# Optimization experiments

Hardware: AMD Instinct MI355X
Metric: run time of the kernel (lower is better)

## Reference

```python
import jax, jax.numpy as jnp
import numpy as np

B, S, D, F, E = 8, 4096, 512, 2048, 8


def setup_inputs() -> dict:
    key = jax.random.key(0)
    ks = jax.random.split(key, 10)
    std = 0.02
    return {
        "x": jax.random.normal(ks[0], (B, S, D), dtype=jnp.float32),
        "gate_w": jax.random.normal(ks[1], (D, E), dtype=jnp.float32) * std,
        "gate_b": jnp.zeros((E,), dtype=jnp.float32),
        "w1": jax.random.normal(ks[2], (E, D, F), dtype=jnp.float32) * std,
        "b1": jnp.zeros((E, F), dtype=jnp.float32),
        "w2": jax.random.normal(ks[3], (E, D, F), dtype=jnp.float32) * std,
        "b2": jnp.zeros((E, F), dtype=jnp.float32),
        "w3": jax.random.normal(ks[4], (E, F, D), dtype=jnp.float32) * std,
        "b3": jnp.zeros((E, D), dtype=jnp.float32),
    }


def reference(x, gate_w, gate_b, w1, b1, w2, b2, w3, b3):
    b, s, d = x.shape
    xt = x.reshape(-1, d)                      # [N, D]
    logits = xt @ gate_w + gate_b              # [N, E]
    top = jnp.argmax(logits, axis=-1)          # [N] top-1 expert per token
    soft = jax.nn.softmax(logits, axis=-1)     # [N, E]
    num_experts = gate_w.shape[1]

    out = jnp.zeros_like(xt)
    # Loop over the small fixed expert set; weight is zero where a token
    # is not routed to expert i, reproducing masked dispatch+combine math.
    for i in range(num_experts):
        h = jax.nn.gelu(xt @ w1[i] + b1[i], approximate=False) * (xt @ w2[i] + b2[i])
        y = h @ w3[i] + b3[i]                  # [N, D]
        w = jnp.where(top == i, soft[:, i], 0.0)[:, None]
        out = out + w * y

    aux_loss = jnp.asarray(0.0, dtype=x.dtype)  # eval mode: no aux loss
    return out.reshape(b, s, d), aux_loss
```

## Files before the change

kernel.cpp:

```cpp
#include <hip/hip_runtime.h>
#include <hip/hip_bf16.h>

typedef unsigned short u16;
typedef __bf16 bf16x8 __attribute__((ext_vector_type(8)));
typedef float f32x4 __attribute__((ext_vector_type(4)));

#define N_TOK 32768
#define DD 512
#define FF 2048
#define EE 8

#define CTL_CNT 0
#define CTL_CUR 8
#define CTL_OFF 16
#define CTL_NT 25
#define CTL_TE 32
#define CTL_TI 304

__device__ inline u16 f2bu(float f) {
  unsigned u = __builtin_bit_cast(unsigned, f);
  unsigned r = (u + 0x7fffu + ((u >> 16) & 1u)) >> 16;
  return (u16)r;
}

__device__ inline f32x4 mfma16(bf16x8 a, bf16x8 b, f32x4 c) {
  return __builtin_amdgcn_mfma_f32_16x16x32_bf16(a, b, c, 0, 0, 0);
}

__device__ inline void gload_lds16(const void* g, void* l) {
  __builtin_amdgcn_global_load_lds(
      (const __attribute__((address_space(1))) void*)g,
      (__attribute__((address_space(3))) void*)l, 16, 0, 0);
}

__device__ inline void stage128x32(u16* lds, const u16* g, int ld) {
  const int t = threadIdx.x;
#pragma unroll
  for (int s = 0; s < 2; ++s) {
    const int e = s * 2048 + t * 8;
    const int row = e >> 5;
    const int kin = e & 31;
    gload_lds16(g + (size_t)row * ld + kin, lds + e);
  }
}

__global__ void gate_k(const float* __restrict__ x, const float* __restrict__ gw,
                       const float* __restrict__ gb, int* __restrict__ eid,
                       float* __restrict__ wgt) {
  __shared__ float gws[DD * EE];
  for (int i = threadIdx.x; i < DD * EE; i += 256) gws[i] = gw[i];
  __syncthreads();
  const int tok = (int)((blockIdx.x * 256 + threadIdx.x) >> 6);
  const int lane = threadIdx.x & 63;
  const float* xr = x + (size_t)tok * DD;
  float a[EE];
#pragma unroll
  for (int e = 0; e < EE; ++e) a[e] = 0.f;
#pragma unroll
  for (int i = 0; i < 8; ++i) {
    const int d = lane + i * 64;
    const float xv = xr[d];
#pragma unroll
    for (int e = 0; e < EE; ++e) a[e] += xv * gws[d * EE + e];
  }
#pragma unroll
  for (int e = 0; e < EE; ++e) {
#pragma unroll
    for (int off = 32; off > 0; off >>= 1) a[e] += __shfl_xor(a[e], off);
  }
  if (lane == 0) {
    float m = -1e30f; int bi = 0;
#pragma unroll
    for (int e = 0; e < EE; ++e) {
      const float l2 = a[e] + gb[e];
      a[e] = l2;
      if (l2 > m) { m = l2; bi = e; }
    }
    float s = 0.f;
#pragma unroll
    for (int e = 0; e < EE; ++e) s += expf(a[e] - m);
    eid[tok] = bi;
    wgt[tok] = 1.f / s;
  }
}

__global__ void count_k(const int* __restrict__ eid, int* __restrict__ ctl) {
  __shared__ int h[EE];
  if (threadIdx.x < EE) h[threadIdx.x] = 0;
  __syncthreads();
  atomicAdd(&h[eid[blockIdx.x * 256 + threadIdx.x]], 1);
  __syncthreads();
  if (threadIdx.x < EE) atomicAdd(&ctl[CTL_CNT + threadIdx.x], h[threadIdx.x]);
}

__global__ void scan_k(int* __restrict__ ctl, float* __restrict__ aux) {
  int o = 0, nt = 0;
  for (int e = 0; e < EE; ++e) {
    ctl[CTL_OFF + e] = o;
    ctl[CTL_CUR + e] = o;
    const int c = ctl[CTL_CNT + e];
    const int t = (c + 127) >> 7;
    for (int i = 0; i < t; ++i) { ctl[CTL_TE + nt] = e; ctl[CTL_TI + nt] = i; ++nt; }
    o += c;
  }
  ctl[CTL_OFF + 8] = o;
  ctl[CTL_NT] = nt;
  *aux = 0.f;
}

__global__ void pos_k(const int* __restrict__ eid, const float* __restrict__ wgt,
                      int* __restrict__ ctl, int* __restrict__ sorted,
                      float* __restrict__ wgt_s) {
  __shared__ int h[EE], base[EE];
  const int t = blockIdx.x * 256 + threadIdx.x;
  if (threadIdx.x < EE) h[threadIdx.x] = 0;
  __syncthreads();
  const int e = eid[t];
  const int r = atomicAdd(&h[e], 1);
  __syncthreads();
  if (threadIdx.x < EE)
    base[threadIdx.x] = atomicAdd(&ctl[CTL_CUR + threadIdx.x], h[threadIdx.x]);
  __syncthreads();
  const int p = base[e] + r;
  sorted[p] = t;
  wgt_s[p] = wgt[t];
}

__global__ void gather_k(const float* __restrict__ x, const int* __restrict__ sorted,
                         u16* __restrict__ Xg) {
  const int p = (int)((blockIdx.x * 256 + threadIdx.x) >> 6);
  const int lane = threadIdx.x & 63;
  const int t = sorted[p];
  const float* src = x + (size_t)t * DD + lane * 8;
  const float4 v0 = *(const float4*)(src);
  const float4 v1 = *(const float4*)(src + 4);
  union { u16 u[8]; uint4 v; } o;
  o.u[0] = f2bu(v0.x); o.u[1] = f2bu(v0.y); o.u[2] = f2bu(v0.z); o.u[3] = f2bu(v0.w);
  o.u[4] = f2bu(v1.x); o.u[5] = f2bu(v1.y); o.u[6] = f2bu(v1.z); o.u[7] = f2bu(v1.w);
  *reinterpret_cast<uint4*>(Xg + (size_t)p * DD + lane * 8) = o.v;
}

__global__ void transp_k(const float* __restrict__ in, u16* __restrict__ out,
                         int R, int C) {
  __shared__ u16 tile[64][66];
  const int e = blockIdx.z;
  const int c0 = blockIdx.x * 64, r0 = blockIdx.y * 64;
  const float* ip = in + (size_t)e * R * C;
  u16* op = out + (size_t)e * R * C;
  const int tx = threadIdx.x & 63, ty = threadIdx.x >> 6;
#pragma unroll
  for (int k = 0; k < 16; ++k) {
    const int r = ty * 16 + k;
    tile[r][tx] = f2bu(ip[(size_t)(r0 + r) * C + c0 + tx]);
  }
  __syncthreads();
#pragma unroll
  for (int k = 0; k < 16; ++k) {
    const int c = ty * 16 + k;
    op[(size_t)(c0 + c) * R + r0 + tx] = tile[tx][c];
  }
}

__global__ __launch_bounds__(256, 2) void gemm1_k(
    const u16* __restrict__ Xg, const u16* __restrict__ W1t,
    const u16* __restrict__ W2t, const float* __restrict__ b1,
    const float* __restrict__ b2, u16* __restrict__ Hbuf,
    const int* __restrict__ ctl) {
  const int bx = blockIdx.x;
  if (bx >= ctl[CTL_NT]) return;
  const int e = ctl[CTL_TE + bx];
  const int ti = ctl[CTL_TI + bx];
  const int cnt = ctl[CTL_CNT + e];
  const int row0 = ctl[CTL_OFF + e] + ti * 128;
  const int rows = min(128, cnt - ti * 128);
  const int n0 = blockIdx.y * 128;

  __shared__ u16 As[2][4096];
  __shared__ u16 B1s[2][4096];
  __shared__ u16 B2s[2][4096];

  const u16* Ab = Xg + (size_t)row0 * DD;
  const u16* B1b = W1t + ((size_t)e * FF + n0) * DD;
  const u16* B2b = W2t + ((size_t)e * FF + n0) * DD;

  const f32x4 z = {0.f, 0.f, 0.f, 0.f};
  f32x4 acc1[4][4], acc2[4][4];
#pragma unroll
  for (int i = 0; i < 4; ++i)
#pragma unroll
    for (int j = 0; j < 4; ++j) { acc1[i][j] = z; acc2[i][j] = z; }

  stage128x32(As[0], Ab, DD);
  stage128x32(B1s[0], B1b, DD);
  stage128x32(B2s[0], B2b, DD);
  asm volatile("s_waitcnt vmcnt(0)" ::: "memory");
  __syncthreads();

  const int lane = threadIdx.x & 63;
  const int w = threadIdx.x >> 6;
  const int wr = w >> 1, wc = w & 1;
  const int ro = (lane & 15) * 32 + (lane >> 4) * 8;

  int cur = 0;
  for (int kt = 0; kt < 16; ++kt) {
    if (kt < 15) {
      stage128x32(As[cur ^ 1], Ab + (kt + 1) * 32, DD);
      stage128x32(B1s[cur ^ 1], B1b + (kt + 1) * 32, DD);
      stage128x32(B2s[cur ^ 1], B2b + (kt + 1) * 32, DD);
    }
    bf16x8 af[4], bf1[4], bf2[4];
#pragma unroll
    for (int mi = 0; mi < 4; ++mi)
      af[mi] = *(const bf16x8*)&As[cur][(wr * 64 + mi * 16) * 32 + ro];
#pragma unroll
    for (int ni = 0; ni < 4; ++ni) {
      bf1[ni] = *(const bf16x8*)&B1s[cur][(wc * 64 + ni * 16) * 32 + ro];
      bf2[ni] = *(const bf16x8*)&B2s[cur][(wc * 64 + ni * 16) * 32 + ro];
    }
#pragma unroll
    for (int mi = 0; mi < 4; ++mi)
#pragma unroll
      for (int ni = 0; ni < 4; ++ni) {
        acc1[mi][ni] = mfma16(af[mi], bf1[ni], acc1[mi][ni]);
        acc2[mi][ni] = mfma16(af[mi], bf2[ni], acc2[mi][ni]);
      }
    asm volatile("s_waitcnt vmcnt(0)" ::: "memory");
    __syncthreads();
    cur ^= 1;
  }

#pragma unroll
  for (int mi = 0; mi < 4; ++mi) {
#pragma unroll
    for (int ni = 0; ni < 4; ++ni) {
      const int c = wc * 64 + ni * 16 + (lane & 15);
      const float bb1 = b1[(size_t)e * FF + n0 + c];
      const float bb2 = b2[(size_t)e * FF + n0 + c];
#pragma unroll
      for (int j = 0; j < 4; ++j) {
        const int r = wr * 64 + mi * 16 + (lane >> 4) * 4 + j;
        if (r < rows) {
          const float v1 = acc1[mi][ni][j] + bb1;
          const float v2 = acc2[mi][ni][j] + bb2;
          const float h = 0.5f * v1 * (1.f + erff(v1 * 0.70710678118f)) * v2;
          Hbuf[(size_t)(row0 + r) * FF + n0 + c] = f2bu(h);
        }
      }
    }
  }
}

__global__ __launch_bounds__(256, 2) void gemm2_k(
    const u16* __restrict__ Hbuf, const u16* __restrict__ W3t,
    const float* __restrict__ b3, const int* __restrict__ sorted,
    const float* __restrict__ wgt_s, float* __restrict__ out,
    const int* __restrict__ ctl) {
  const int bx = blockIdx.x;
  if (bx >= ctl[CTL_NT]) return;
  const int e = ctl[CTL_TE + bx];
  const int ti = ctl[CTL_TI + bx];
  const int cnt = ctl[CTL_CNT + e];
  const int row0 = ctl[CTL_OFF + e] + ti * 128;
  const int rows = min(128, cnt - ti * 128);
  const int n0 = blockIdx.y * 128;

  __shared__ u16 As[2][4096];
  __shared__ u16 Bs[2][4096];
  const u16* Ab = Hbuf + (size_t)row0 * FF;
  const u16* Bb = W3t + ((size_t)e * DD + n0) * FF;

  const f32x4 z = {0.f, 0.f, 0.f, 0.f};
  f32x4 acc[4][4];
#pragma unroll
  for (int i = 0; i < 4; ++i)
#pragma unroll
    for (int j = 0; j < 4; ++j) acc[i][j] = z;

  stage128x32(As[0], Ab, FF);
  stage128x32(Bs[0], Bb, FF);
  asm volatile("s_waitcnt vmcnt(0)" ::: "memory");
  __syncthreads();

  const int lane = threadIdx.x & 63;
  const int w = threadIdx.x >> 6;
  const int wr = w >> 1, wc = w & 1;
  const int ro = (lane & 15) * 32 + (lane >> 4) * 8;

  int cur = 0;
  for (int kt = 0; kt < 64; ++kt) {
    if (kt < 63) {
      stage128x32(As[cur ^ 1], Ab + (kt + 1) * 32, FF);
      stage128x32(Bs[cur ^ 1], Bb + (kt + 1) * 32, FF);
    }
    bf16x8 af[4], bf[4];
#pragma unroll
    for (int mi = 0; mi < 4; ++mi)
      af[mi] = *(const bf16x8*)&As[cur][(wr * 64 + mi * 16) * 32 + ro];
#pragma unroll
    for (int ni = 0; ni < 4; ++ni)
      bf[ni] = *(const bf16x8*)&Bs[cur][(wc * 64 + ni * 16) * 32 + ro];
#pragma unroll
    for (int mi = 0; mi < 4; ++mi)
#pragma unroll
      for (int ni = 0; ni < 4; ++ni)
        acc[mi][ni] = mfma16(af[mi], bf[ni], acc[mi][ni]);
    asm volatile("s_waitcnt vmcnt(0)" ::: "memory");
    __syncthreads();
    cur ^= 1;
  }

#pragma unroll
  for (int mi = 0; mi < 4; ++mi) {
#pragma unroll
    for (int ni = 0; ni < 4; ++ni) {
      const int c = wc * 64 + ni * 16 + (lane & 15);
      const float bb3 = b3[(size_t)e * DD + n0 + c];
#pragma unroll
      for (int j = 0; j < 4; ++j) {
        const int r = wr * 64 + mi * 16 + (lane >> 4) * 4 + j;
        if (r < rows) {
          const int p = row0 + r;
          const int tok = sorted[p];
          out[(size_t)tok * DD + n0 + c] = wgt_s[p] * (acc[mi][ni][j] + bb3);
        }
      }
    }
  }
}

extern "C" void kernel_launch(void* const* d_in, const int* in_sizes, int n_in,
                              void* d_out, int out_size, void* d_ws, size_t ws_size,
                              hipStream_t stream) {
  const float* x  = (const float*)d_in[0];
  const float* gw = (const float*)d_in[1];
  const float* gb = (const float*)d_in[2];
  const float* w1 = (const float*)d_in[3];
  const float* b1 = (const float*)d_in[4];
  const float* w2 = (const float*)d_in[5];
  const float* b2 = (const float*)d_in[6];
  const float* w3 = (const float*)d_in[7];
  const float* b3 = (const float*)d_in[8];
  float* out = (float*)d_out;

  char* base = (char*)d_ws;
  size_t off = 0;
  auto take = [&](size_t bytes) {
    char* r = base + off;
    off += (bytes + 255) & ~(size_t)255;
    return r;
  };
  int*   ctl    = (int*)take(4096);
  int*   eid    = (int*)take((size_t)N_TOK * 4);
  float* wgt    = (float*)take((size_t)N_TOK * 4);
  int*   sorted = (int*)take((size_t)(N_TOK + 128) * 4);
  float* wgt_s  = (float*)take((size_t)(N_TOK + 128) * 4);
  u16*   Xg     = (u16*)take((size_t)(N_TOK + 128) * DD * 2);
  u16*   W1t    = (u16*)take((size_t)EE * FF * DD * 2);
  u16*   W2t    = (u16*)take((size_t)EE * FF * DD * 2);
  u16*   W3t    = (u16*)take((size_t)EE * DD * FF * 2);
  u16*   Hbuf   = (u16*)take((size_t)(N_TOK + 128) * FF * 2);

  hipMemsetAsync(ctl, 0, 64, stream);

  gate_k<<<8192, 256, 0, stream>>>(x, gw, gb, eid, wgt);
  count_k<<<128, 256, 0, stream>>>(eid, ctl);
  scan_k<<<1, 1, 0, stream>>>(ctl, out + (size_t)N_TOK * DD);
  pos_k<<<128, 256, 0, stream>>>(eid, wgt, ctl, sorted, wgt_s);
  gather_k<<<8192, 256, 0, stream>>>(x, sorted, Xg);

  transp_k<<<dim3(32, 8, EE), 256, 0, stream>>>(w1, W1t, 512, 2048);
  transp_k<<<dim3(32, 8, EE), 256, 0, stream>>>(w2, W2t, 512, 2048);
  transp_k<<<dim3(8, 32, EE), 256, 0, stream>>>(w3, W3t, 2048, 512);

  gemm1_k<<<dim3(264, 16), 256, 0, stream>>>(Xg, W1t, W2t, b1, b2, Hbuf, ctl);
  gemm2_k<<<dim3(264, 4), 256, 0, stream>>>(Hbuf, W3t, b3, sorted, wgt_s, out, ctl);
}
```

Before: 664.1 us.

## Fuse bf16 cast into gate, gather rows in GEMM, swizzle LDS tiles

The fp32-to-bf16 conversion of x now happens inside the gate kernel, which removes the separate gather kernel. gemm1 instead indexes rows through the sorted permutation while staging its A tiles. Both GEMMs use an XOR-swizzled LDS layout, paired with remapped global-load addresses, to cut bank conflicts on the bf16x8 fragment reads. The gate weights in shared memory are padded to stride 9, and the tile table in scan is built in parallel across 256 threads. The trade-off is that gemm1 now reads scattered rows, giving less coalescing on its A loads.

```diff
diff --git a/kernel.cpp b/kernel.cpp
--- a/kernel.cpp
+++ b/kernel.cpp
@@ -33,26 +33,25 @@
       (__attribute__((address_space(3))) void*)l, 16, 0, 0);
 }
 
-__device__ inline void stage128x32(u16* lds, const u16* g, int ld) {
-  const int t = threadIdx.x;
-#pragma unroll
-  for (int s = 0; s < 2; ++s) {
-    const int e = s * 2048 + t * 8;
-    const int row = e >> 5;
-    const int kin = e & 31;
-    gload_lds16(g + (size_t)row * ld + kin, lds + e);
-  }
-}
 
 __global__ void gate_k(const float* __restrict__ x, const float* __restrict__ gw,
                        const float* __restrict__ gb, int* __restrict__ eid,
-                       float* __restrict__ wgt) {
-  __shared__ float gws[DD * EE];
-  for (int i = threadIdx.x; i < DD * EE; i += 256) gws[i] = gw[i];
+                       float* __restrict__ wgt, u16* __restrict__ Xb) {
+  __shared__ float gws[DD * 9];
+  for (int i = threadIdx.x; i < DD * EE; i += 256)
+    gws[(i >> 3) * 9 + (i & 7)] = gw[i];
   __syncthreads();
   const int tok = (int)((blockIdx.x * 256 + threadIdx.x) >> 6);
   const int lane = threadIdx.x & 63;
   const float* xr = x + (size_t)tok * DD;
+
+  const float4 v0 = *(const float4*)(xr + lane * 8);
+  const float4 v1 = *(const float4*)(xr + lane * 8 + 4);
+  union { u16 u[8]; uint4 v; } o;
+  o.u[0] = f2bu(v0.x); o.u[1] = f2bu(v0.y); o.u[2] = f2bu(v0.z); o.u[3] = f2bu(v0.w);
+  o.u[4] = f2bu(v1.x); o.u[5] = f2bu(v1.y); o.u[6] = f2bu(v1.z); o.u[7] = f2bu(v1.w);
+  *reinterpret_cast<uint4*>(Xb + (size_t)tok * DD + lane * 8) = o.v;
+
   float a[EE];
 #pragma unroll
   for (int e = 0; e < EE; ++e) a[e] = 0.f;
@@ -61,7 +60,7 @@
     const int d = lane + i * 64;
     const float xv = xr[d];
 #pragma unroll
-    for (int e = 0; e < EE; ++e) a[e] += xv * gws[d * EE + e];
+    for (int e = 0; e < EE; ++e) a[e] += xv * gws[d * 9 + e];
   }
 #pragma unroll
   for (int e = 0; e < EE; ++e) {
@@ -94,18 +93,30 @@
 }
 
 __global__ void scan_k(int* __restrict__ ctl, float* __restrict__ aux) {
-  int o = 0, nt = 0;
-  for (int e = 0; e < EE; ++e) {
-    ctl[CTL_OFF + e] = o;
-    ctl[CTL_CUR + e] = o;
-    const int c = ctl[CTL_CNT + e];
-    const int t = (c + 127) >> 7;
-    for (int i = 0; i < t; ++i) { ctl[CTL_TE + nt] = e; ctl[CTL_TI + nt] = i; ++nt; }
-    o += c;
-  }
-  ctl[CTL_OFF + 8] = o;
-  ctl[CTL_NT] = nt;
-  *aux = 0.f;
+  __shared__ int tstart[EE + 1];
+  if (threadIdx.x == 0) {
+    int o = 0, nt = 0;
+    for (int e = 0; e < EE; ++e) {
+      ctl[CTL_OFF + e] = o;
+      ctl[CTL_CUR + e] = o;
+      tstart[e] = nt;
+      const int c = ctl[CTL_CNT + e];
+      nt += (c + 127) >> 7;
+      o += c;
+    }
+    tstart[EE] = nt;
+    ctl[CTL_OFF + 8] = o;
+    ctl[CTL_NT] = nt;
+    *aux = 0.f;
+  }
+  __syncthreads();
+  const int nt = tstart[EE];
+  for (int i = threadIdx.x; i < nt; i += 256) {
+    int e = 0;
+    while (tstart[e + 1] <= i) ++e;
+    ctl[CTL_TE + i] = e;
+    ctl[CTL_TI + i] = i - tstart[e];
+  }
 }
 
 __global__ void pos_k(const int* __restrict__ eid, const float* __restrict__ wgt,
@@ -124,20 +135,6 @@
   const int p = base[e] + r;
   sorted[p] = t;
   wgt_s[p] = wgt[t];
-}
-
-__global__ void gather_k(const float* __restrict__ x, const int* __restrict__ sorted,
-                         u16* __restrict__ Xg) {
-  const int p = (int)((blockIdx.x * 256 + threadIdx.x) >> 6);
-  const int lane = threadIdx.x & 63;
-  const int t = sorted[p];
-  const float* src = x + (size_t)t * DD + lane * 8;
-  const float4 v0 = *(const float4*)(src);
-  const float4 v1 = *(const float4*)(src + 4);
-  union { u16 u[8]; uint4 v; } o;
-  o.u[0] = f2bu(v0.x); o.u[1] = f2bu(v0.y); o.u[2] = f2bu(v0.z); o.u[3] = f2bu(v0.w);
-  o.u[4] = f2bu(v1.x); o.u[5] = f2bu(v1.y); o.u[6] = f2bu(v1.z); o.u[7] = f2bu(v1.w);
-  *reinterpret_cast<uint4*>(Xg + (size_t)p * DD + lane * 8) = o.v;
 }
 
 __global__ void transp_k(const float* __restrict__ in, u16* __restrict__ out,
@@ -162,10 +159,10 @@
 }
 
 __global__ __launch_bounds__(256, 2) void gemm1_k(
-    const u16* __restrict__ Xg, const u16* __restrict__ W1t,
+    const u16* __restrict__ Xb, const u16* __restrict__ W1t,
     const u16* __restrict__ W2t, const float* __restrict__ b1,
     const float* __restrict__ b2, u16* __restrict__ Hbuf,
-    const int* __restrict__ ctl) {
+    const int* __restrict__ sorted, const int* __restrict__ ctl) {
   const int bx = blockIdx.x;
   if (bx >= ctl[CTL_NT]) return;
   const int e = ctl[CTL_TE + bx];
@@ -179,10 +176,32 @@
   __shared__ u16 B1s[2][4096];
   __shared__ u16 B2s[2][4096];
 
-  const u16* Ab = Xg + (size_t)row0 * DD;
   const u16* B1b = W1t + ((size_t)e * FF + n0) * DD;
   const u16* B2b = W2t + ((size_t)e * FF + n0) * DD;
 
+  const int t = threadIdx.x;
+  const u16 *aSrc[2], *b1Src[2], *b2Src[2];
+  int dofs[2];
+#pragma unroll
+  for (int s = 0; s < 2; ++s) {
+    const int Gp = s * 256 + t;
+    const int r = ((Gp >> 3) << 1) | (((Gp >> 2) ^ (Gp >> 4)) & 1);
+    const int g = (Gp & 3) ^ (r & 3);
+    dofs[s] = Gp * 8;
+    const int idx = min(row0 + r, N_TOK - 1);
+    aSrc[s]  = Xb + (size_t)sorted[idx] * DD + g * 8;
+    b1Src[s] = B1b + (size_t)r * DD + g * 8;
+    b2Src[s] = B2b + (size_t)r * DD + g * 8;
+  }
+  auto stage_all = [&](int buf, int kc) {
+#pragma unroll
+    for (int s = 0; s < 2; ++s) gload_lds16(aSrc[s] + kc, &As[buf][dofs[s]]);
+#pragma unroll
+    for (int s = 0; s < 2; ++s) gload_lds16(b1Src[s] + kc, &B1s[buf][dofs[s]]);
+#pragma unroll
+    for (int s = 0; s < 2; ++s) gload_lds16(b2Src[s] + kc, &B2s[buf][dofs[s]]);
+  };
+
   const f32x4 z = {0.f, 0.f, 0.f, 0.f};
   f32x4 acc1[4][4], acc2[4][4];
 #pragma unroll
@@ -190,32 +209,32 @@
 #pragma unroll
     for (int j = 0; j < 4; ++j) { acc1[i][j] = z; acc2[i][j] = z; }
 
-  stage128x32(As[0], Ab, DD);
-  stage128x32(B1s[0], B1b, DD);
-  stage128x32(B2s[0], B2b, DD);
+  stage_all(0, 0);
   asm volatile("s_waitcnt vmcnt(0)" ::: "memory");
   __syncthreads();
 
   const int lane = threadIdx.x & 63;
-  const int w = threadIdx.x >> 6;
+  const int w = t >> 6;
   const int wr = w >> 1, wc = w & 1;
-  const int ro = (lane & 15) * 32 + (lane >> 4) * 8;
+  const int l15 = lane & 15, g8 = (lane >> 4) * 8, xv = (lane & 7) << 3;
+  int offA[4], offB[4];
+#pragma unroll
+  for (int i = 0; i < 4; ++i) {
+    offA[i] = (((wr * 64 + i * 16 + l15) * 32 + g8) ^ xv);
+    offB[i] = (((wc * 64 + i * 16 + l15) * 32 + g8) ^ xv);
+  }
 
   int cur = 0;
   for (int kt = 0; kt < 16; ++kt) {
-    if (kt < 15) {
-      stage128x32(As[cur ^ 1], Ab + (kt + 1) * 32, DD);
-      stage128x32(B1s[cur ^ 1], B1b + (kt + 1) * 32, DD);
-      stage128x32(B2s[cur ^ 1], B2b + (kt + 1) * 32, DD);
-    }
+    if (kt < 15) stage_all(cur ^ 1, (kt + 1) * 32);
     bf16x8 af[4], bf1[4], bf2[4];
 #pragma unroll
     for (int mi = 0; mi < 4; ++mi)
-      af[mi] = *(const bf16x8*)&As[cur][(wr * 64 + mi * 16) * 32 + ro];
+      af[mi] = *(const bf16x8*)&As[cur][offA[mi]];
 #pragma unroll
     for (int ni = 0; ni < 4; ++ni) {
-      bf1[ni] = *(const bf16x8*)&B1s[cur][(wc * 64 + ni * 16) * 32 + ro];
-      bf2[ni] = *(const bf16x8*)&B2s[cur][(wc * 64 + ni * 16) * 32 + ro];
+      bf1[ni] = *(const bf16x8*)&B1s[cur][offB[ni]];
+      bf2[ni] = *(const bf16x8*)&B2s[cur][offB[ni]];
     }
 #pragma unroll
     for (int mi = 0; mi < 4; ++mi)
@@ -269,6 +288,25 @@
   const u16* Ab = Hbuf + (size_t)row0 * FF;
   const u16* Bb = W3t + ((size_t)e * DD + n0) * FF;
 
+  const int t = threadIdx.x;
+  const u16 *aSrc[2], *bSrc[2];
+  int dofs[2];
+#pragma unroll
+  for (int s = 0; s < 2; ++s) {
+    const int Gp = s * 256 + t;
+    const int r = ((Gp >> 3) << 1) | (((Gp >> 2) ^ (Gp >> 4)) & 1);
+    const int g = (Gp & 3) ^ (r & 3);
+    dofs[s] = Gp * 8;
+    aSrc[s] = Ab + (size_t)r * FF + g * 8;
+    bSrc[s] = Bb + (size_t)r * FF + g * 8;
+  }
+  auto stage_all = [&](int buf, int kc) {
+#pragma unroll
+    for (int s = 0; s < 2; ++s) gload_lds16(aSrc[s] + kc, &As[buf][dofs[s]]);
+#pragma unroll
+    for (int s = 0; s < 2; ++s) gload_lds16(bSrc[s] + kc, &Bs[buf][dofs[s]]);
+  };
+
   const f32x4 z = {0.f, 0.f, 0.f, 0.f};
   f32x4 acc[4][4];
 #pragma unroll
@@ -276,29 +314,31 @@
 #pragma unroll
     for (int j = 0; j < 4; ++j) acc[i][j] = z;
 
-  stage128x32(As[0], Ab, FF);
-  stage128x32(Bs[0], Bb, FF);
+  stage_all(0, 0);
   asm volatile("s_waitcnt vmcnt(0)" ::: "memory");
   __syncthreads();
 
   const int lane = threadIdx.x & 63;
-  const int w = threadIdx.x >> 6;
+  const int w = t >> 6;
   const int wr = w >> 1, wc = w & 1;
-  const int ro = (lane & 15) * 32 + (lane >> 4) * 8;
+  const int l15 = lane & 15, g8 = (lane >> 4) * 8, xv = (lane & 7) << 3;
+  int offA[4], offB[4];
+#pragma unroll
+  for (int i = 0; i < 4; ++i) {
+    offA[i] = (((wr * 64 + i * 16 + l15) * 32 + g8) ^ xv);
+    offB[i] = (((wc * 64 + i * 16 + l15) * 32 + g8) ^ xv);
+  }
 
   int cur = 0;
   for (int kt = 0; kt < 64; ++kt) {
-    if (kt < 63) {
-      stage128x32(As[cur ^ 1], Ab + (kt + 1) * 32, FF);
-      stage128x32(Bs[cur ^ 1], Bb + (kt + 1) * 32, FF);
-    }
+    if (kt < 63) stage_all(cur ^ 1, (kt + 1) * 32);
     bf16x8 af[4], bf[4];
 #pragma unroll
     for (int mi = 0; mi < 4; ++mi)
-      af[mi] = *(const bf16x8*)&As[cur][(wr * 64 + mi * 16) * 32 + ro];
+      af[mi] = *(const bf16x8*)&As[cur][offA[mi]];
 #pragma unroll
     for (int ni = 0; ni < 4; ++ni)
-      bf[ni] = *(const bf16x8*)&Bs[cur][(wc * 64 + ni * 16) * 32 + ro];
+      bf[ni] = *(const bf16x8*)&Bs[cur][offB[ni]];
 #pragma unroll
     for (int mi = 0; mi < 4; ++mi)
 #pragma unroll
@@ -354,7 +394,7 @@
   float* wgt    = (float*)take((size_t)N_TOK * 4);
   int*   sorted = (int*)take((size_t)(N_TOK + 128) * 4);
   float* wgt_s  = (float*)take((size_t)(N_TOK + 128) * 4);
-  u16*   Xg     = (u16*)take((size_t)(N_TOK + 128) * DD * 2);
+  u16*   Xb     = (u16*)take((size_t)N_TOK * DD * 2);
   u16*   W1t    = (u16*)take((size_t)EE * FF * DD * 2);
   u16*   W2t    = (u16*)take((size_t)EE * FF * DD * 2);
   u16*   W3t    = (u16*)take((size_t)EE * DD * FF * 2);
@@ -362,16 +402,15 @@
 
   hipMemsetAsync(ctl, 0, 64, stream);
 
-  gate_k<<<8192, 256, 0, stream>>>(x, gw, gb, eid, wgt);
+  gate_k<<<8192, 256, 0, stream>>>(x, gw, gb, eid, wgt, Xb);
   count_k<<<128, 256, 0, stream>>>(eid, ctl);
-  scan_k<<<1, 1, 0, stream>>>(ctl, out + (size_t)N_TOK * DD);
+  scan_k<<<1, 256, 0, stream>>>(ctl, out + (size_t)N_TOK * DD);
   pos_k<<<128, 256, 0, stream>>>(eid, wgt, ctl, sorted, wgt_s);
-  gather_k<<<8192, 256, 0, stream>>>(x, sorted, Xg);
 
   transp_k<<<dim3(32, 8, EE), 256, 0, stream>>>(w1, W1t, 512, 2048);
   transp_k<<<dim3(32, 8, EE), 256, 0, stream>>>(w2, W2t, 512, 2048);
   transp_k<<<dim3(8, 32, EE), 256, 0, stream>>>(w3, W3t, 2048, 512);
 
-  gemm1_k<<<dim3(264, 16), 256, 0, stream>>>(Xg, W1t, W2t, b1, b2, Hbuf, ctl);
+  gemm1_k<<<dim3(264, 16), 256, 0, stream>>>(Xb, W1t, W2t, b1, b2, Hbuf, sorted, ctl);
   gemm2_k<<<dim3(264, 4), 256, 0, stream>>>(Hbuf, W3t, b3, sorted, wgt_s, out, ctl);
 }
```

Measured after the change: 620.0 us. 6.6% less time.
